# Kernel optimization log

Hardware: AMD Instinct MI355X
Metric: run time of the kernel (lower is better)

The kernel has to match this reference:

```python
import jax, jax.numpy as jnp
import numpy as np


def setup_inputs() -> dict:
    key = jax.random.key(0)
    ks = jax.random.split(key, 5)
    B, T, D, U, O = 128, 512, 512, 1024, 512
    x = jax.random.normal(ks[0], (B, T, D), dtype=jnp.float32)
    h0 = jnp.zeros((B, U), dtype=jnp.float32)
    c0 = jnp.zeros((B, U), dtype=jnp.float32)
    # Keras LSTMCell params: kernel [D,4U], recurrent_kernel [U,4U], bias [4U]; gate order i,f,g,o
    kernel = jax.random.normal(ks[1], (D, 4 * U), dtype=jnp.float32) * (1.0 / np.sqrt(D))
    rec_kernel = jax.random.normal(ks[2], (U, 4 * U), dtype=jnp.float32) * (1.0 / np.sqrt(U))
    bias = jnp.zeros((4 * U,), dtype=jnp.float32)
    Wd = jax.random.normal(ks[3], (U, O), dtype=jnp.float32) * (1.0 / np.sqrt(U))
    bd = jnp.zeros((O,), dtype=jnp.float32)
    return {"x": x, "h0": h0, "c0": c0, "kernel": kernel, "rec_kernel": rec_kernel,
            "bias": bias, "Wd": Wd, "bd": bd}


def _lstm_decode(x, h0, c0, kernel, rec_kernel, bias, Wd, bd):
    U = h0.shape[-1]
    # Precompute input contribution for all timesteps in one big GEMM: [B,T,4U]
    xz = jnp.einsum("btd,dg->btg", x, kernel) + bias

    def step(carry, xz_t):
        h, c = carry
        z = xz_t + h @ rec_kernel                     # [B,4U]
        i, f, g, o = jnp.split(z, 4, axis=-1)         # Keras gate order i,f,g,o
        i = jax.nn.sigmoid(i)
        f = jax.nn.sigmoid(f)
        o = jax.nn.sigmoid(o)
        c = f * c + i * jnp.tanh(g)
        h = o * jnp.tanh(c)
        return (h, c), h

    (_, _), hs = jax.lax.scan(step, (h0, c0), jnp.swapaxes(xz, 0, 1))  # hs: [T,B,U]
    hs = jnp.swapaxes(hs, 0, 1)                       # [B,T,U]
    # Per-step dense projection (output_layer of BasicDecoder)
    return jnp.einsum("btu,uo->bto", hs, Wd) + bd


def reference(x, h0, c0, kernel, rec_kernel, bias, Wd, bd):
    return _lstm_decode(x, h0, c0, kernel, rec_kernel, bias, Wd, bd)
```

## Files before the change

### kernel.cpp

```cpp
#include <hip/hip_runtime.h>
#include <hip/hip_bf16.h>

#define B_   128
#define T_   512
#define D_   512
#define U_   1024
#define O_   512
#define K_   1536
#define G4U_ 4096
#define NBLK 256
#define APITCH 1544

typedef __attribute__((ext_vector_type(8))) short short8;
typedef __attribute__((ext_vector_type(4))) float f32x4;
typedef __attribute__((ext_vector_type(4))) int int4v;

__device__ __align__(16) unsigned short g_xbf[(size_t)B_ * T_ * D_];
__device__ __align__(16) unsigned short g_Wt[(size_t)G4U_ * K_];
__device__ __align__(16) unsigned short g_Wdt[(size_t)O_ * U_];
__device__ __align__(16) unsigned short g_hall[(size_t)(T_ + 1) * B_ * U_];
__device__ unsigned int g_flag[NBLK * 32];

__device__ __forceinline__ unsigned short f2b(float f) {
  unsigned u = __float_as_uint(f);
  u += 0x7fffu + ((u >> 16) & 1u);
  return (unsigned short)(u >> 16);
}

__global__ void prep_kernel(const float* __restrict__ x, const float* __restrict__ h0,
                            const float* __restrict__ kern, const float* __restrict__ rkern,
                            const float* __restrict__ Wd) {
  size_t tid = (size_t)blockIdx.x * blockDim.x + threadIdx.x;
  size_t np  = (size_t)gridDim.x * blockDim.x;
  if (tid < NBLK * 32) g_flag[tid] = 0u;

  const size_t nx8 = (size_t)B_ * T_ * D_ / 8;
  const float4* xv = (const float4*)x;
  for (size_t i = tid; i < nx8; i += np) {
    float4 v0 = xv[2 * i], v1 = xv[2 * i + 1];
    unsigned short tmp[8];
    tmp[0] = f2b(v0.x); tmp[1] = f2b(v0.y); tmp[2] = f2b(v0.z); tmp[3] = f2b(v0.w);
    tmp[4] = f2b(v1.x); tmp[5] = f2b(v1.y); tmp[6] = f2b(v1.z); tmp[7] = f2b(v1.w);
    *(int4*)&g_xbf[i * 8] = *(const int4*)tmp;
  }

  const size_t nw = (size_t)G4U_ * (K_ / 8);
  for (size_t i = tid; i < nw; i += np) {
    size_t cg = i / (K_ / 8);
    int kb = (int)(i % (K_ / 8)) * 8;
    int c = (int)(cg >> 6), g = (int)((cg >> 4) & 3), j = (int)(cg & 15);
    int n = g * 1024 + (c << 4) + j;
    unsigned short tmp[8];
#pragma unroll
    for (int q = 0; q < 8; ++q) {
      int k = kb + q;
      float v = (k < 512) ? kern[(size_t)k * G4U_ + n] : rkern[(size_t)(k - 512) * G4U_ + n];
      tmp[q] = f2b(v);
    }
    *(int4*)&g_Wt[cg * K_ + kb] = *(const int4*)tmp;
  }

  const size_t nd = (size_t)O_ * (U_ / 8);
  for (size_t i = tid; i < nd; i += np) {
    int o  = (int)(i >> 7);
    int ub = (int)(i & 127) * 8;
    unsigned short tmp[8];
#pragma unroll
    for (int q = 0; q < 8; ++q) tmp[q] = f2b(Wd[(size_t)(ub + q) * O_ + o]);
    *(int4*)&g_Wdt[(size_t)o * U_ + ub] = *(const int4*)tmp;
  }

  const size_t nh = (size_t)B_ * U_;
  for (size_t i = tid; i < nh; i += np) g_hall[i] = f2b(h0[i]);
}

__global__ __launch_bounds__(256, 1) void lstm_kernel(const float* __restrict__ c0,
                                                      const float* __restrict__ bias,
                                                      const float* __restrict__ bd,
                                                      float* __restrict__ out) {
  const int b    = blockIdx.x;
  const int tid  = threadIdx.x;
  const int wq   = tid >> 6;
  const int lane = tid & 63;
  const int rg   = lane >> 4;
  const int fr   = lane & 15;

  const int mg = b >> 6;
  const int m0 = mg * 32;
  const int ug = b & 63;
  const int u0 = ug * 16;

  __shared__ __align__(16) unsigned short Ast[32 * APITCH];
  __shared__ f32x4 zpo[4][32][17];
  __shared__ float po[4][16][20];

  short8 wz[12][4];
#pragma unroll
  for (int kt = 0; kt < 12; ++kt)
#pragma unroll
    for (int g = 0; g < 4; ++g)
      wz[kt][g] = *(const short8*)&g_Wt[(size_t)(ug * 64 + g * 16 + fr) * K_ +
                                        wq * 384 + kt * 32 + rg * 8];

  const int oc0 = (ug >> 1) * 16;
  const int orh = (ug & 1) * 16;
  short8 wd[8];
#pragma unroll
  for (int kt = 0; kt < 8; ++kt)
    wd[kt] = *(const short8*)&g_Wdt[(size_t)(oc0 + fr) * U_ + wq * 256 + kt * 32 + rg * 8];

  const int erow = tid >> 3;
  const int euu  = (tid & 7) * 2;
  float cv[2];
  f32x4 bv[2];
#pragma unroll
  for (int j = 0; j < 2; ++j) {
    cv[j] = c0[(size_t)(m0 + erow) * U_ + u0 + euu + j];
    f32x4 tv;
#pragma unroll
    for (int g = 0; g < 4; ++g) tv[g] = bias[g * 1024 + u0 + euu + j];
    bv[j] = tv;
  }

  const int orow = tid >> 4, ocl = tid & 15;
  const float bd_v = bd[oc0 + ocl];

  const unsigned short* az0p = &Ast[(size_t)fr * APITCH + wq * 384 + rg * 8];
  const unsigned short* az1p = az0p + 16 * APITCH;
  const unsigned short* aop  = &Ast[(size_t)(orh + fr) * APITCH + 512 + wq * 256 + rg * 8];

  const int sr = tid >> 3, sc = tid & 7;

  {
    const unsigned short* sx = &g_xbf[((size_t)(m0 + sr) * T_ + 0) * D_];
    int4v bx[8];
#pragma unroll
    for (int q = 0; q < 8; ++q) bx[q] = *(const int4v*)&sx[q * 64 + sc * 8];
#pragma unroll
    for (int q = 0; q < 8; ++q) *(int4v*)&Ast[(size_t)sr * APITCH + q * 64 + sc * 8] = bx[q];
  }

  for (int t = 0; t <= T_; ++t) {
    if (t > 0 && tid < 64) {
      unsigned int* fp = &g_flag[(mg * 64 + tid) * 32];
      while (__hip_atomic_load(fp, __ATOMIC_RELAXED, __HIP_MEMORY_SCOPE_AGENT) <
             (unsigned)t)
        __builtin_amdgcn_s_sleep(1);
    }
    __syncthreads();

    {
      const unsigned short* hc = &g_hall[(size_t)t * (B_ * U_)];
      int4v bh[16];
#pragma unroll
      for (int q = 0; q < 16; ++q)
        bh[q] = *(const int4v*)&hc[(size_t)(m0 + sr) * U_ + q * 64 + sc * 8];
#pragma unroll
      for (int q = 0; q < 16; ++q)
        *(int4v*)&Ast[(size_t)sr * APITCH + 512 + q * 64 + sc * 8] = bh[q];
    }
    __syncthreads();

    if (t < T_) {
      f32x4 acc[2][4];
#pragma unroll
      for (int rt = 0; rt < 2; ++rt)
#pragma unroll
        for (int g = 0; g < 4; ++g) acc[rt][g] = (f32x4){0.f, 0.f, 0.f, 0.f};
#pragma unroll
      for (int kt = 0; kt < 12; ++kt) {
        short8 a0 = *(const short8*)&az0p[kt * 32];
        short8 a1 = *(const short8*)&az1p[kt * 32];
#pragma unroll
        for (int g = 0; g < 4; ++g) {
          acc[0][g] = __builtin_amdgcn_mfma_f32_16x16x32_bf16(a0, wz[kt][g], acc[0][g], 0, 0, 0);
          acc[1][g] = __builtin_amdgcn_mfma_f32_16x16x32_bf16(a1, wz[kt][g], acc[1][g], 0, 0, 0);
        }
      }
#pragma unroll
      for (int rt = 0; rt < 2; ++rt)
#pragma unroll
        for (int r = 0; r < 4; ++r) {
          f32x4 v = {acc[rt][0][r], acc[rt][1][r], acc[rt][2][r], acc[rt][3][r]};
          zpo[wq][rt * 16 + rg * 4 + r][fr] = v;
        }
      __syncthreads();

      {
        unsigned short* hn = &g_hall[(size_t)(t + 1) * (B_ * U_)];
        float hv[2];
#pragma unroll
        for (int j = 0; j < 2; ++j) {
          f32x4 z = zpo[0][erow][euu + j] + zpo[1][erow][euu + j] +
                    zpo[2][erow][euu + j] + zpo[3][erow][euu + j];
          z += bv[j];
          float ig = 1.f / (1.f + __expf(-z[0]));
          float fg = 1.f / (1.f + __expf(-z[1]));
          float gg = tanhf(z[2]);
          float og = 1.f / (1.f + __expf(-z[3]));
          cv[j] = fg * cv[j] + ig * gg;
          hv[j] = og * tanhf(cv[j]);
        }
        unsigned int pk = (unsigned)f2b(hv[0]) | ((unsigned)f2b(hv[1]) << 16);
        *(volatile unsigned int*)&hn[(size_t)(m0 + erow) * U_ + u0 + euu] = pk;
      }
      __syncthreads();

      if (tid == 0)
        __hip_atomic_store(&g_flag[b * 32], (unsigned)(t + 1), __ATOMIC_RELAXED,
                           __HIP_MEMORY_SCOPE_AGENT);

      if (t + 1 < T_) {
        const unsigned short* sx = &g_xbf[((size_t)(m0 + sr) * T_ + (t + 1)) * D_];
        int4v bx[8];
#pragma unroll
        for (int q = 0; q < 8; ++q) bx[q] = *(const int4v*)&sx[q * 64 + sc * 8];
#pragma unroll
        for (int q = 0; q < 8; ++q) *(int4v*)&Ast[(size_t)sr * APITCH + q * 64 + sc * 8] = bx[q];
      }
    }

    if (t > 0) {
      f32x4 oa = {0.f, 0.f, 0.f, 0.f};
#pragma unroll
      for (int kt = 0; kt < 8; ++kt)
        oa = __builtin_amdgcn_mfma_f32_16x16x32_bf16(*(const short8*)&aop[kt * 32],
                                                     wd[kt], oa, 0, 0, 0);
#pragma unroll
      for (int r = 0; r < 4; ++r) po[wq][rg * 4 + r][fr] = oa[r];
      __syncthreads();
      float v = po[0][orow][ocl] + po[1][orow][ocl] + po[2][orow][ocl] +
                po[3][orow][ocl] + bd_v;
      out[((size_t)(m0 + orh + orow) * T_ + (t - 1)) * O_ + oc0 + ocl] = v;
    }
  }
}

extern "C" void kernel_launch(void* const* d_in, const int* in_sizes, int n_in,
                              void* d_out, int out_size, void* d_ws, size_t ws_size,
                              hipStream_t stream) {
  const float* x    = (const float*)d_in[0];
  const float* h0   = (const float*)d_in[1];
  const float* c0   = (const float*)d_in[2];
  const float* kern = (const float*)d_in[3];
  const float* rk   = (const float*)d_in[4];
  const float* bias = (const float*)d_in[5];
  const float* Wd   = (const float*)d_in[6];
  const float* bd   = (const float*)d_in[7];
  float* out = (float*)d_out;
  (void)in_sizes; (void)n_in; (void)d_ws; (void)ws_size; (void)out_size;

  prep_kernel<<<dim3(1024), dim3(256), 0, stream>>>(x, h0, kern, rk, Wd);
  lstm_kernel<<<dim3(NBLK), dim3(256), 0, stream>>>(c0, bias, bd, out);
}
```

Before: 2.761 ms.

## Overlap input-projection MFMAs with barrier wait and load operands directly to registers

Splits the fused x/h GEMM so that the x-part MFMAs for the current step run before the cross-block flag wait, hiding part of the compute behind synchronisation. It drops the shared-memory A staging buffer and one __syncthreads, loading h and x fragments straight from global into MFMA operand registers. It also remaps block indices so that each batch-row group's 64 cooperating blocks share an XCD-parity pattern, aiming at better L2 locality for the h exchange. The price is higher register pressure and redundant global reads of h (the output projection reloads h from global), plus reliance on the hardware's XCD dispatch order.

```diff
diff --git a/kernel.cpp b/kernel.cpp
--- a/kernel.cpp
+++ b/kernel.cpp
@@ -9,7 +9,6 @@
 #define K_   1536
 #define G4U_ 4096
 #define NBLK 256
-#define APITCH 1544
 
 typedef __attribute__((ext_vector_type(8))) short short8;
 typedef __attribute__((ext_vector_type(4))) float f32x4;
@@ -85,22 +84,30 @@
   const int rg   = lane >> 4;
   const int fr   = lane & 15;
 
-  const int mg = b >> 6;
-  const int m0 = mg * 32;
-  const int ug = b & 63;
-  const int u0 = ug * 16;
-
-  __shared__ __align__(16) unsigned short Ast[32 * APITCH];
+  const int xcd = b & 7, idx = b >> 3;
+  const int mg  = xcd >> 1;
+  const int sl  = idx * 2 + (xcd & 1);
+  const int lb  = mg * 64 + sl;
+  const int m0  = mg * 32;
+  const int ug  = sl;
+  const int u0  = ug * 16;
+
   __shared__ f32x4 zpo[4][32][17];
   __shared__ float po[4][16][20];
 
-  short8 wz[12][4];
-#pragma unroll
-  for (int kt = 0; kt < 12; ++kt)
+  short8 wzx[4][4], wzh[8][4];
+#pragma unroll
+  for (int kt = 0; kt < 4; ++kt)
 #pragma unroll
     for (int g = 0; g < 4; ++g)
-      wz[kt][g] = *(const short8*)&g_Wt[(size_t)(ug * 64 + g * 16 + fr) * K_ +
-                                        wq * 384 + kt * 32 + rg * 8];
+      wzx[kt][g] = *(const short8*)&g_Wt[(size_t)(ug * 64 + g * 16 + fr) * K_ +
+                                         wq * 128 + kt * 32 + rg * 8];
+#pragma unroll
+  for (int kt = 0; kt < 8; ++kt)
+#pragma unroll
+    for (int g = 0; g < 4; ++g)
+      wzh[kt][g] = *(const short8*)&g_Wt[(size_t)(ug * 64 + g * 16 + fr) * K_ +
+                                         512 + wq * 256 + kt * 32 + rg * 8];
 
   const int oc0 = (ug >> 1) * 16;
   const int orh = (ug & 1) * 16;
@@ -125,22 +132,36 @@
   const int orow = tid >> 4, ocl = tid & 15;
   const float bd_v = bd[oc0 + ocl];
 
-  const unsigned short* az0p = &Ast[(size_t)fr * APITCH + wq * 384 + rg * 8];
-  const unsigned short* az1p = az0p + 16 * APITCH;
-  const unsigned short* aop  = &Ast[(size_t)(orh + fr) * APITCH + 512 + wq * 256 + rg * 8];
-
-  const int sr = tid >> 3, sc = tid & 7;
-
+  const int hcol = wq * 256 + rg * 8;
+  const int xcol = wq * 128 + rg * 8;
+
+  short8 axf0[4], axf1[4];
   {
-    const unsigned short* sx = &g_xbf[((size_t)(m0 + sr) * T_ + 0) * D_];
-    int4v bx[8];
-#pragma unroll
-    for (int q = 0; q < 8; ++q) bx[q] = *(const int4v*)&sx[q * 64 + sc * 8];
-#pragma unroll
-    for (int q = 0; q < 8; ++q) *(int4v*)&Ast[(size_t)sr * APITCH + q * 64 + sc * 8] = bx[q];
+    const unsigned short* x0 = &g_xbf[((size_t)(m0 + fr) * T_ + 0) * D_ + xcol];
+    const unsigned short* x1 = &g_xbf[((size_t)(m0 + 16 + fr) * T_ + 0) * D_ + xcol];
+#pragma unroll
+    for (int kt = 0; kt < 4; ++kt) {
+      axf0[kt] = *(const short8*)&x0[kt * 32];
+      axf1[kt] = *(const short8*)&x1[kt * 32];
+    }
   }
 
   for (int t = 0; t <= T_; ++t) {
+    f32x4 acc[2][4];
+    if (t < T_) {
+#pragma unroll
+      for (int rt = 0; rt < 2; ++rt)
+#pragma unroll
+        for (int g = 0; g < 4; ++g) acc[rt][g] = (f32x4){0.f, 0.f, 0.f, 0.f};
+#pragma unroll
+      for (int kt = 0; kt < 4; ++kt)
+#pragma unroll
+        for (int g = 0; g < 4; ++g) {
+          acc[0][g] = __builtin_amdgcn_mfma_f32_16x16x32_bf16(axf0[kt], wzx[kt][g], acc[0][g], 0, 0, 0);
+          acc[1][g] = __builtin_amdgcn_mfma_f32_16x16x32_bf16(axf1[kt], wzx[kt][g], acc[1][g], 0, 0, 0);
+        }
+    }
+
     if (t > 0 && tid < 64) {
       unsigned int* fp = &g_flag[(mg * 64 + tid) * 32];
       while (__hip_atomic_load(fp, __ATOMIC_RELAXED, __HIP_MEMORY_SCOPE_AGENT) <
@@ -149,34 +170,23 @@
     }
     __syncthreads();
 
-    {
-      const unsigned short* hc = &g_hall[(size_t)t * (B_ * U_)];
-      int4v bh[16];
-#pragma unroll
-      for (int q = 0; q < 16; ++q)
-        bh[q] = *(const int4v*)&hc[(size_t)(m0 + sr) * U_ + q * 64 + sc * 8];
-#pragma unroll
-      for (int q = 0; q < 16; ++q)
-        *(int4v*)&Ast[(size_t)sr * APITCH + 512 + q * 64 + sc * 8] = bh[q];
-    }
-    __syncthreads();
-
     if (t < T_) {
-      f32x4 acc[2][4];
-#pragma unroll
-      for (int rt = 0; rt < 2; ++rt)
-#pragma unroll
-        for (int g = 0; g < 4; ++g) acc[rt][g] = (f32x4){0.f, 0.f, 0.f, 0.f};
-#pragma unroll
-      for (int kt = 0; kt < 12; ++kt) {
-        short8 a0 = *(const short8*)&az0p[kt * 32];
-        short8 a1 = *(const short8*)&az1p[kt * 32];
+      const unsigned short* hc  = &g_hall[(size_t)t * (B_ * U_)];
+      const unsigned short* h0p = &hc[(size_t)(m0 + fr) * U_ + hcol];
+      const unsigned short* h1p = &hc[(size_t)(m0 + 16 + fr) * U_ + hcol];
+      short8 ha0[8], ha1[8];
+#pragma unroll
+      for (int kt = 0; kt < 8; ++kt) ha0[kt] = *(const short8*)&h0p[kt * 32];
+#pragma unroll
+      for (int kt = 0; kt < 8; ++kt) ha1[kt] = *(const short8*)&h1p[kt * 32];
+#pragma unroll
+      for (int kt = 0; kt < 8; ++kt)
 #pragma unroll
         for (int g = 0; g < 4; ++g) {
-          acc[0][g] = __builtin_amdgcn_mfma_f32_16x16x32_bf16(a0, wz[kt][g], acc[0][g], 0, 0, 0);
-          acc[1][g] = __builtin_amdgcn_mfma_f32_16x16x32_bf16(a1, wz[kt][g], acc[1][g], 0, 0, 0);
-        }
-      }
+          acc[0][g] = __builtin_amdgcn_mfma_f32_16x16x32_bf16(ha0[kt], wzh[kt][g], acc[0][g], 0, 0, 0);
+          acc[1][g] = __builtin_amdgcn_mfma_f32_16x16x32_bf16(ha1[kt], wzh[kt][g], acc[1][g], 0, 0, 0);
+        }
+
 #pragma unroll
       for (int rt = 0; rt < 2; ++rt)
 #pragma unroll
@@ -207,25 +217,30 @@
       __syncthreads();
 
       if (tid == 0)
-        __hip_atomic_store(&g_flag[b * 32], (unsigned)(t + 1), __ATOMIC_RELAXED,
+        __hip_atomic_store(&g_flag[lb * 32], (unsigned)(t + 1), __ATOMIC_RELAXED,
                            __HIP_MEMORY_SCOPE_AGENT);
 
       if (t + 1 < T_) {
-        const unsigned short* sx = &g_xbf[((size_t)(m0 + sr) * T_ + (t + 1)) * D_];
-        int4v bx[8];
-#pragma unroll
-        for (int q = 0; q < 8; ++q) bx[q] = *(const int4v*)&sx[q * 64 + sc * 8];
-#pragma unroll
-        for (int q = 0; q < 8; ++q) *(int4v*)&Ast[(size_t)sr * APITCH + q * 64 + sc * 8] = bx[q];
+        const unsigned short* x0 = &g_xbf[((size_t)(m0 + fr) * T_ + (t + 1)) * D_ + xcol];
+        const unsigned short* x1 = &g_xbf[((size_t)(m0 + 16 + fr) * T_ + (t + 1)) * D_ + xcol];
+#pragma unroll
+        for (int kt = 0; kt < 4; ++kt) {
+          axf0[kt] = *(const short8*)&x0[kt * 32];
+          axf1[kt] = *(const short8*)&x1[kt * 32];
+        }
       }
     }
 
     if (t > 0) {
+      const unsigned short* ho = &g_hall[(size_t)t * (B_ * U_) +
+                                         (size_t)(m0 + orh + fr) * U_ + hcol];
+      short8 hov[8];
+#pragma unroll
+      for (int kt = 0; kt < 8; ++kt) hov[kt] = *(const short8*)&ho[kt * 32];
       f32x4 oa = {0.f, 0.f, 0.f, 0.f};
 #pragma unroll
       for (int kt = 0; kt < 8; ++kt)
-        oa = __builtin_amdgcn_mfma_f32_16x16x32_bf16(*(const short8*)&aop[kt * 32],
-                                                     wd[kt], oa, 0, 0, 0);
+        oa = __builtin_amdgcn_mfma_f32_16x16x32_bf16(hov[kt], wd[kt], oa, 0, 0, 0);
 #pragma unroll
       for (int r = 0; r < 4; ++r) po[wq][rg * 4 + r][fr] = oa[r];
       __syncthreads();
```

New measurement: 3.664 ms. +32.7%, slower.
